# Performance work log

Measured on AMD Instinct MI355X. Metric: run time of the kernel, lower is better.

Reference implementation:

```python
import jax, jax.numpy as jnp
import numpy as np

B, C, N, K = 2, 64, 20000, 16
COUT = 64


def setup_inputs() -> dict:
    key = jax.random.key(0)
    k1, k2, k3, k4, k5 = jax.random.split(key, 5)
    x = jax.random.normal(k1, (B, C, N, 1), dtype=jnp.float32)
    edge_index = jax.random.randint(k2, (2, B, N, K), 0, N)
    pos = jax.random.normal(k3, (B, 3, N, 1), dtype=jnp.float32)
    # BasicConv([2C, COUT]) -> 1x1 Conv2d weight [COUT, 2C] (+bias), then ReLU
    W = jax.random.normal(k4, (COUT, 2 * C), dtype=jnp.float32) * (1.0 / np.sqrt(2 * C))
    b = jax.random.normal(k5, (COUT,), dtype=jnp.float32) * 0.01
    return {"x": x, "edge_index": edge_index, "pos": pos, "W": W, "b": b}


def _gather(t, idx):
    # t: [B, C, N, 1], idx: [B, N, K] -> [B, C, N, K]
    t3 = t[..., 0]  # [B, C, N]
    return jax.vmap(lambda tb, ib: tb[:, ib])(t3, idx)


def reference(x, edge_index, pos, W, b):
    x_i = _gather(x, edge_index[1])           # [B, C, N, K] center
    x_j = _gather(x, edge_index[0])           # [B, C, N, K] neighbor
    feat = jnp.concatenate([x_i, x_j - x_i], axis=1)  # [B, 2C, N, K]
    # 1x1 conv + bias + ReLU
    out = jnp.einsum('oc,bcnk->bonk', W, feat) + b[None, :, None, None]
    out = jax.nn.relu(out)
    # distance-based suppression
    pos_i = _gather(pos, edge_index[1])       # [B, 3, N, K]
    pos_j = _gather(pos, edge_index[0])
    dis = jnp.sqrt(jnp.sum(jnp.square(pos_j - pos_i), axis=1))  # [B, N, K]
    suppression = 2.0 * jax.nn.sigmoid(-dis)[:, None, :, :]     # [B, 1, N, K]
    out = out * suppression
    max_value = jnp.max(out, axis=-1, keepdims=True)             # [B, COUT, N, 1]
    return max_value
```

## Files before the change

kernel.cpp:

```cpp
#include <hip/hip_runtime.h>
#include <math.h>

#define B_    2
#define C_    64
#define N_    20000
#define K_    16
#define COUT_ 64
#define TN1   64
#define NB1   ((N_ + TN1 - 1) / TN1)
#define TN2   16
#define NB2   (N_ / TN2)

typedef unsigned int   u32;
typedef unsigned short u16;

static __device__ __forceinline__ u16 f2bf(float f) {
    union { float f; u32 u; } v; v.f = f;
    u32 r = (v.u + 0x7FFFu + ((v.u >> 16) & 1u)) >> 16;
    return (u16)r;
}
static __device__ __forceinline__ float uasf(u32 u) {
    union { u32 u; float f; } v; v.u = u; return v.f;
}

__global__ __launch_bounds__(256)
void stage1(const float* __restrict__ x, const float* __restrict__ W,
            const float* __restrict__ bias,
            u16* __restrict__ zbuf, u16* __restrict__ ybuf) {
    __shared__ float xt[64][68];
    __shared__ float wc[64][130];

    const int bi   = blockIdx.x;
    const int b    = bi / NB1;
    const int n0   = (bi % NB1) * TN1;
    const int t    = threadIdx.x;
    const int lane = t & 63;
    const int w    = t >> 6;

    #pragma unroll
    for (int r = 0; r < 16; ++r) {
        int flat = r * 256 + t;
        int o = flat >> 6, c = flat & 63;
        float w1 = W[o * 128 + c];
        float w2 = W[o * 128 + 64 + c];
        wc[c][2 * o]     = w1 - w2;
        wc[c][2 * o + 1] = w2;
    }
    const float* xb = x + (size_t)b * C_ * N_;
    #pragma unroll
    for (int r = 0; r < 4; ++r) {
        int flat = r * 256 + t;
        int c = flat >> 4, ng = (flat & 15) * 4;
        int n = n0 + ng;
        float4 v;
        if (n + 3 < N_) {
            v = *(const float4*)&xb[c * N_ + n];
        } else {
            v.x = (n     < N_) ? xb[c * N_ + n    ] : 0.0f;
            v.y = (n + 1 < N_) ? xb[c * N_ + n + 1] : 0.0f;
            v.z = (n + 2 < N_) ? xb[c * N_ + n + 2] : 0.0f;
            v.w = (n + 3 < N_) ? xb[c * N_ + n + 3] : 0.0f;
        }
        *(float4*)&xt[c][ng] = v;
    }
    const float bo = bias[lane];
    __syncthreads();

    const int nb = w * 16;
    float4 z0 = {bo,bo,bo,bo}, z1 = z0, z2 = z0, z3 = z0;
    float4 y0 = {0,0,0,0},     y1 = y0, y2 = y0, y3 = y0;

#define FMA4(ZR, YR, XV) \
    ZR.x = fmaf(wv.x, XV.x, ZR.x);  YR.x = fmaf(wv.y, XV.x, YR.x); \
    ZR.y = fmaf(wv.x, XV.y, ZR.y);  YR.y = fmaf(wv.y, XV.y, YR.y); \
    ZR.z = fmaf(wv.x, XV.z, ZR.z);  YR.z = fmaf(wv.y, XV.z, YR.z); \
    ZR.w = fmaf(wv.x, XV.w, ZR.w);  YR.w = fmaf(wv.y, XV.w, YR.w);

    #pragma unroll 2
    for (int c = 0; c < 64; ++c) {
        float2 wv = *(const float2*)&wc[c][2 * lane];
        float4 xa = *(const float4*)&xt[c][nb];
        float4 xv1 = *(const float4*)&xt[c][nb + 4];
        float4 xv2 = *(const float4*)&xt[c][nb + 8];
        float4 xv3 = *(const float4*)&xt[c][nb + 12];
        FMA4(z0, y0, xa)
        FMA4(z1, y1, xv1)
        FMA4(z2, y2, xv2)
        FMA4(z3, y3, xv3)
    }
#undef FMA4

    {
        const size_t rowb = (size_t)b * N_;
        auto st = [&](int i, float zv, float yv) {
            int n = n0 + nb + i;
            if (n < N_) {
                size_t off = (rowb + n) * 64 + lane;
                zbuf[off] = f2bf(zv);
                ybuf[off] = f2bf(yv);
            }
        };
        st(0,  z0.x, y0.x); st(1,  z0.y, y0.y); st(2,  z0.z, y0.z); st(3,  z0.w, y0.w);
        st(4,  z1.x, y1.x); st(5,  z1.y, y1.y); st(6,  z1.z, y1.z); st(7,  z1.w, y1.w);
        st(8,  z2.x, y2.x); st(9,  z2.y, y2.y); st(10, z2.z, y2.z); st(11, z2.w, y2.w);
        st(12, z3.x, y3.x); st(13, z3.y, y3.y); st(14, z3.z, y3.z); st(15, z3.w, y3.w);
    }
}

__global__ __launch_bounds__(256)
void stage2(const int* __restrict__ ei, const float* __restrict__ pos,
            const u16* __restrict__ zbuf, const u16* __restrict__ ybuf,
            float* __restrict__ out) {
    __shared__ uint2 esl[TN2][17];
    __shared__ float tile[TN2][66];

    const int bi   = blockIdx.x;
    const int b    = bi / NB2;
    const int n0   = (bi % NB2) * TN2;
    const int t    = threadIdx.x;
    const int nl   = t >> 4;
    const int kh   = (t >> 3) & 1;
    const int cq   = t & 7;

    {
        const int    idx = n0 * K_ + t;
        const int*   e0  = ei + (size_t)b * N_ * K_;
        const int*   e1  = ei + ((size_t)B_ + b) * N_ * K_;
        const float* pb  = pos + (size_t)b * 3 * N_;
        int i0 = e0[idx], i1 = e1[idx];
        float dx = pb[i0]          - pb[i1];
        float dy = pb[N_ + i0]     - pb[N_ + i1];
        float dz = pb[2 * N_ + i0] - pb[2 * N_ + i1];
        float dis = sqrtf(dx * dx + dy * dy + dz * dz);
        float s = 2.0f / (1.0f + __expf(dis));
        esl[t >> 4][t & 15] = make_uint2((u32)i0 | ((u32)i1 << 16),
                                         __float_as_uint(s));
    }
    __syncthreads();

    const u16* zb = zbuf + (size_t)b * N_ * 64;
    const u16* yb = ybuf + (size_t)b * N_ * 64;

    float4 ma = {0,0,0,0}, mb = {0,0,0,0};

#define COMB(ZW, YW, MLO, MHI) { \
    float zl = uasf((ZW) << 16), zh = uasf((ZW) & 0xFFFF0000u); \
    float yl = uasf((YW) << 16), yh = uasf((YW) & 0xFFFF0000u); \
    MLO = fmaxf(MLO, fmaxf(zl + yl, 0.0f) * s); \
    MHI = fmaxf(MHI, fmaxf(zh + yh, 0.0f) * s); }

    #pragma unroll
    for (int i = 0; i < 8; ++i) {
        int   k = 2 * i + kh;
        uint2 e = esl[nl][k];
        int   i0 = (int)(e.x & 0xFFFFu);
        int   i1 = (int)(e.x >> 16);
        float s  = uasf(e.y);
        uint4 z4 = *((const uint4*)(zb + ((size_t)i1 << 6)) + cq);
        uint4 y4 = *((const uint4*)(yb + ((size_t)i0 << 6)) + cq);
        COMB(z4.x, y4.x, ma.x, ma.y)
        COMB(z4.y, y4.y, ma.z, ma.w)
        COMB(z4.z, y4.z, mb.x, mb.y)
        COMB(z4.w, y4.w, mb.z, mb.w)
    }
#undef COMB

    ma.x = fmaxf(ma.x, __shfl_xor(ma.x, 8));
    ma.y = fmaxf(ma.y, __shfl_xor(ma.y, 8));
    ma.z = fmaxf(ma.z, __shfl_xor(ma.z, 8));
    ma.w = fmaxf(ma.w, __shfl_xor(ma.w, 8));
    mb.x = fmaxf(mb.x, __shfl_xor(mb.x, 8));
    mb.y = fmaxf(mb.y, __shfl_xor(mb.y, 8));
    mb.z = fmaxf(mb.z, __shfl_xor(mb.z, 8));
    mb.w = fmaxf(mb.w, __shfl_xor(mb.w, 8));

    if (kh == 0) {
        int cb = cq * 8;
        *(float2*)&tile[nl][cb]     = make_float2(ma.x, ma.y);
        *(float2*)&tile[nl][cb + 2] = make_float2(ma.z, ma.w);
        *(float2*)&tile[nl][cb + 4] = make_float2(mb.x, mb.y);
        *(float2*)&tile[nl][cb + 6] = make_float2(mb.z, mb.w);
    }
    __syncthreads();

    #pragma unroll
    for (int r = 0; r < 4; ++r) {
        int flat = r * 256 + t;
        int o = flat >> 4, n2 = flat & 15;
        __builtin_nontemporal_store(tile[n2][o],
            &out[((size_t)b * COUT_ + o) * N_ + n0 + n2]);
    }
}

extern "C" void kernel_launch(void* const* d_in, const int* in_sizes, int n_in,
                              void* d_out, int out_size, void* d_ws, size_t ws_size,
                              hipStream_t stream) {
    const float* x    = (const float*)d_in[0];
    const int*   ei   = (const int*)  d_in[1];
    const float* pos  = (const float*)d_in[2];
    const float* W    = (const float*)d_in[3];
    const float* bias = (const float*)d_in[4];
    float*       out  = (float*)d_out;

    const size_t tabElems = (size_t)B_ * N_ * 64;
    u16* zbuf = (u16*)d_ws;
    u16* ybuf = zbuf + tabElems;

    hipLaunchKernelGGL(stage1, dim3(B_ * NB1), dim3(256), 0, stream,
                       x, W, bias, zbuf, ybuf);
    hipLaunchKernelGGL(stage2, dim3(B_ * NB2), dim3(256), 0, stream,
                       ei, pos, zbuf, ybuf, out);
}
```

Measured before the change: 109.5 us.

## Split gather tables into channel chunks to shrink per-pass working set

Stage1 now writes the bf16 z/y tables in four 16-channel chunk planes instead of one 64-channel row per point. Stage2 launches one block per chunk, point tile and batch, and gathers only 32-byte rows from one chunk, so each pass works on a smaller table that fits better in cache for the random neighbor gathers. The cost is that the edge indices and the position-based suppression are recomputed four times, once per chunk. The point tile is also enlarged, with the reduction shuffles and the output write adjusted to match.

```diff
diff --git a/kernel.cpp b/kernel.cpp
--- a/kernel.cpp
+++ b/kernel.cpp
@@ -6,9 +6,10 @@
 #define N_    20000
 #define K_    16
 #define COUT_ 64
+#define NCH   4
 #define TN1   64
 #define NB1   ((N_ + TN1 - 1) / TN1)
-#define TN2   16
+#define TN2   32
 #define NB2   (N_ / TN2)
 
 typedef unsigned int   u32;
@@ -91,11 +92,12 @@
 #undef FMA4
 
     {
-        const size_t rowb = (size_t)b * N_;
+        const size_t cbase = ((size_t)b * NCH + (lane >> 4)) * N_;
+        const int    ci    = lane & 15;
         auto st = [&](int i, float zv, float yv) {
             int n = n0 + nb + i;
             if (n < N_) {
-                size_t off = (rowb + n) * 64 + lane;
+                size_t off = (cbase + n) * 16 + ci;
                 zbuf[off] = f2bf(zv);
                 ybuf[off] = f2bf(yv);
             }
@@ -112,34 +114,40 @@
             const u16* __restrict__ zbuf, const u16* __restrict__ ybuf,
             float* __restrict__ out) {
     __shared__ uint2 esl[TN2][17];
-    __shared__ float tile[TN2][66];
-
-    const int bi   = blockIdx.x;
-    const int b    = bi / NB2;
-    const int n0   = (bi % NB2) * TN2;
-    const int t    = threadIdx.x;
-    const int nl   = t >> 4;
-    const int kh   = (t >> 3) & 1;
-    const int cq   = t & 7;
+    __shared__ float tile[TN2][20];
+
+    const int bi = blockIdx.x;
+    const int c  = bi / (B_ * NB2);
+    const int r  = bi % (B_ * NB2);
+    const int b  = r / NB2;
+    const int n0 = (r % NB2) * TN2;
+    const int t  = threadIdx.x;
+    const int nl = t >> 3;
+    const int kh = (t >> 1) & 3;
+    const int cq = t & 1;
 
     {
-        const int    idx = n0 * K_ + t;
-        const int*   e0  = ei + (size_t)b * N_ * K_;
-        const int*   e1  = ei + ((size_t)B_ + b) * N_ * K_;
-        const float* pb  = pos + (size_t)b * 3 * N_;
-        int i0 = e0[idx], i1 = e1[idx];
-        float dx = pb[i0]          - pb[i1];
-        float dy = pb[N_ + i0]     - pb[N_ + i1];
-        float dz = pb[2 * N_ + i0] - pb[2 * N_ + i1];
-        float dis = sqrtf(dx * dx + dy * dy + dz * dz);
-        float s = 2.0f / (1.0f + __expf(dis));
-        esl[t >> 4][t & 15] = make_uint2((u32)i0 | ((u32)i1 << 16),
-                                         __float_as_uint(s));
+        const int*   e0 = ei + (size_t)b * N_ * K_;
+        const int*   e1 = ei + ((size_t)B_ + b) * N_ * K_;
+        const float* pb = pos + (size_t)b * 3 * N_;
+        #pragma unroll
+        for (int r2 = 0; r2 < 2; ++r2) {
+            int li  = r2 * 256 + t;
+            int idx = n0 * K_ + li;
+            int i0 = e0[idx], i1 = e1[idx];
+            float dx = pb[i0]          - pb[i1];
+            float dy = pb[N_ + i0]     - pb[N_ + i1];
+            float dz = pb[2 * N_ + i0] - pb[2 * N_ + i1];
+            float dis = sqrtf(dx * dx + dy * dy + dz * dz);
+            float s = 2.0f / (1.0f + __expf(dis));
+            esl[li >> 4][li & 15] = make_uint2((u32)i0 | ((u32)i1 << 16),
+                                               __float_as_uint(s));
+        }
     }
     __syncthreads();
 
-    const u16* zb = zbuf + (size_t)b * N_ * 64;
-    const u16* yb = ybuf + (size_t)b * N_ * 64;
+    const u16* zb = zbuf + ((size_t)b * NCH + c) * N_ * 16;
+    const u16* yb = ybuf + ((size_t)b * NCH + c) * N_ * 16;
 
     float4 ma = {0,0,0,0}, mb = {0,0,0,0};
 
@@ -150,14 +158,14 @@
     MHI = fmaxf(MHI, fmaxf(zh + yh, 0.0f) * s); }
 
     #pragma unroll
-    for (int i = 0; i < 8; ++i) {
-        int   k = 2 * i + kh;
+    for (int i = 0; i < 4; ++i) {
+        int   k = 4 * i + kh;
         uint2 e = esl[nl][k];
         int   i0 = (int)(e.x & 0xFFFFu);
         int   i1 = (int)(e.x >> 16);
         float s  = uasf(e.y);
-        uint4 z4 = *((const uint4*)(zb + ((size_t)i1 << 6)) + cq);
-        uint4 y4 = *((const uint4*)(yb + ((size_t)i0 << 6)) + cq);
+        uint4 z4 = *(const uint4*)(zb + (size_t)i1 * 16 + cq * 8);
+        uint4 y4 = *(const uint4*)(yb + (size_t)i0 * 16 + cq * 8);
         COMB(z4.x, y4.x, ma.x, ma.y)
         COMB(z4.y, y4.y, ma.z, ma.w)
         COMB(z4.z, y4.z, mb.x, mb.y)
@@ -165,30 +173,27 @@
     }
 #undef COMB
 
-    ma.x = fmaxf(ma.x, __shfl_xor(ma.x, 8));
-    ma.y = fmaxf(ma.y, __shfl_xor(ma.y, 8));
-    ma.z = fmaxf(ma.z, __shfl_xor(ma.z, 8));
-    ma.w = fmaxf(ma.w, __shfl_xor(ma.w, 8));
-    mb.x = fmaxf(mb.x, __shfl_xor(mb.x, 8));
-    mb.y = fmaxf(mb.y, __shfl_xor(mb.y, 8));
-    mb.z = fmaxf(mb.z, __shfl_xor(mb.z, 8));
-    mb.w = fmaxf(mb.w, __shfl_xor(mb.w, 8));
+#define R4(V, ST) \
+    V.x = fmaxf(V.x, __shfl_xor(V.x, ST)); \
+    V.y = fmaxf(V.y, __shfl_xor(V.y, ST)); \
+    V.z = fmaxf(V.z, __shfl_xor(V.z, ST)); \
+    V.w = fmaxf(V.w, __shfl_xor(V.w, ST));
+    R4(ma, 2)  R4(mb, 2)
+    R4(ma, 4)  R4(mb, 4)
+#undef R4
 
     if (kh == 0) {
-        int cb = cq * 8;
-        *(float2*)&tile[nl][cb]     = make_float2(ma.x, ma.y);
-        *(float2*)&tile[nl][cb + 2] = make_float2(ma.z, ma.w);
-        *(float2*)&tile[nl][cb + 4] = make_float2(mb.x, mb.y);
-        *(float2*)&tile[nl][cb + 6] = make_float2(mb.z, mb.w);
+        *(float4*)&tile[nl][cq * 8]     = ma;
+        *(float4*)&tile[nl][cq * 8 + 4] = mb;
     }
     __syncthreads();
 
     #pragma unroll
-    for (int r = 0; r < 4; ++r) {
-        int flat = r * 256 + t;
-        int o = flat >> 4, n2 = flat & 15;
+    for (int r2 = 0; r2 < 2; ++r2) {
+        int flat = r2 * 256 + t;
+        int o = flat >> 5, n2 = flat & 31;
         __builtin_nontemporal_store(tile[n2][o],
-            &out[((size_t)b * COUT_ + o) * N_ + n0 + n2]);
+            &out[((size_t)b * COUT_ + c * 16 + o) * N_ + n0 + n2]);
     }
 }
 
@@ -202,12 +207,12 @@
     const float* bias = (const float*)d_in[4];
     float*       out  = (float*)d_out;
 
-    const size_t tabElems = (size_t)B_ * N_ * 64;
+    const size_t tabElems = (size_t)B_ * NCH * N_ * 16;
     u16* zbuf = (u16*)d_ws;
     u16* ybuf = zbuf + tabElems;
 
     hipLaunchKernelGGL(stage1, dim3(B_ * NB1), dim3(256), 0, stream,
                        x, W, bias, zbuf, ybuf);
-    hipLaunchKernelGGL(stage2, dim3(B_ * NB2), dim3(256), 0, stream,
+    hipLaunchKernelGGL(stage2, dim3(NCH * B_ * NB2), dim3(256), 0, stream,
                        ei, pos, zbuf, ybuf, out);
 }
```

New measurement: 160.5 us. 46.6% more time.
